# Optimization experiments

Measured on AMD Instinct MI355X. Metric: run time of the kernel, lower is better.

Reference implementation:

```python
import jax, jax.numpy as jnp
import numpy as np

VOCAB = 100000
DIM = 128
BATCH = 65536
N_NEG = 10


def setup_inputs() -> dict:
    key = jax.random.key(0)
    k1, k2, k3, k4, k5 = jax.random.split(key, 5)
    return {
        "pos_u": jax.random.randint(k1, (BATCH,), 0, VOCAB),
        "pos_v": jax.random.randint(k2, (BATCH,), 0, VOCAB),
        "neg_v": jax.random.randint(k3, (BATCH, N_NEG), 0, VOCAB),
        "u_weight": 0.01 * jax.random.normal(k4, (VOCAB, DIM), dtype=jnp.float32),
        "v_weight": 0.01 * jax.random.normal(k5, (VOCAB, DIM), dtype=jnp.float32),
    }


def reference(pos_u, pos_v, neg_v, u_weight, v_weight):
    emb_u = u_weight[pos_u]            # [B, D]
    emb_v = v_weight[pos_v]            # [B, D]
    emb_neg_v = v_weight[neg_v]        # [B, N, D]

    score = jnp.sum(emb_u * emb_v, axis=1)
    score = jnp.clip(score, -10.0, 10.0)
    score = -jax.nn.log_sigmoid(score)           # [B]

    neg_dots = jnp.einsum("bd,bnd->bn", emb_u, emb_neg_v)  # [B, N]
    # NOTE: faithful to source: neg term is ADDED (not negated) to the loss
    neg_score = jnp.sum(jax.nn.log_sigmoid(-neg_dots), axis=1)  # [B]

    return jnp.mean(score + neg_score)
```

## Files before the change

### kernel.cpp

```cpp
#include <hip/hip_runtime.h>
#include <hip/hip_fp8.h>

#define VOCAB 100000
#define DIM 128
#define BATCH 65536
#define N_NEG 10

#define BLOCKS (BATCH / 64)
#define QSCALE 256.0f
#define QINV   (1.0f / 256.0f)

typedef float v4f __attribute__((ext_vector_type(4)));
typedef int   v4i __attribute__((ext_vector_type(4)));
typedef int   v2i __attribute__((ext_vector_type(2)));
typedef float v2f __attribute__((ext_vector_type(2)));

#if __has_builtin(__builtin_amdgcn_cvt_pk_fp8_f32) && __has_builtin(__builtin_amdgcn_cvt_pk_f32_fp8)
__device__ __forceinline__ unsigned int pack4_fp8(float a, float b, float c, float d) {
    int r = __builtin_amdgcn_cvt_pk_fp8_f32(a, b, 0, false);
    r = __builtin_amdgcn_cvt_pk_fp8_f32(c, d, r, true);
    return (unsigned int)r;
}
#else
__device__ __forceinline__ unsigned int pack4_fp8(float a, float b, float c, float d) {
    unsigned int r =  (unsigned int)__hip_fp8_e4m3(a).__x;
    r |= (unsigned int)__hip_fp8_e4m3(b).__x << 8;
    r |= (unsigned int)__hip_fp8_e4m3(c).__x << 16;
    r |= (unsigned int)__hip_fp8_e4m3(d).__x << 24;
    return r;
}
#endif

#if __has_builtin(__builtin_amdgcn_cvt_pk_f32_fp8)
__device__ __forceinline__ void fma4_fp8(float& s, unsigned int x, const float* u) {
    v2f lo = __builtin_amdgcn_cvt_pk_f32_fp8(x, false);
    v2f hi = __builtin_amdgcn_cvt_pk_f32_fp8(x, true);
    s += u[0] * lo.x + u[1] * lo.y + u[2] * hi.x + u[3] * hi.y;
}
#else
__device__ __forceinline__ float fp8_to_f(unsigned int b) {
    __hip_fp8_e4m3 t; t.__x = (__hip_fp8_storage_t)b; return (float)t;
}
__device__ __forceinline__ void fma4_fp8(float& s, unsigned int x, const float* u) {
    s += u[0] * fp8_to_f(x & 0xffu) + u[1] * fp8_to_f((x >> 8) & 0xffu)
       + u[2] * fp8_to_f((x >> 16) & 0xffu) + u[3] * fp8_to_f(x >> 24);
}
#endif

__device__ __forceinline__ float dot16_fp8(uint4 w, const float* uf) {
    float s = 0.0f;
    fma4_fp8(s, w.x, uf + 0);
    fma4_fp8(s, w.y, uf + 4);
    fma4_fp8(s, w.z, uf + 8);
    fma4_fp8(s, w.w, uf + 12);
    return s;
}

__device__ __forceinline__ float softplus_log2(float x) {
    const float y = x * 1.44269504f;
    const float t = __builtin_amdgcn_exp2f(-fabsf(y));
    return fmaxf(y, 0.0f) + __builtin_amdgcn_logf(1.0f + t);
}

__global__ void zero_out_kernel(float* out) { out[0] = 0.0f; }

__global__ __launch_bounds__(256) void quantize_v_kernel(
    const float4* __restrict__ in, uint4* __restrict__ out, float* __restrict__ loss_out) {
    const int i = blockIdx.x * 256 + threadIdx.x;
    if (i == 0) loss_out[0] = 0.0f;
    const float4 a = in[i * 4 + 0];
    const float4 b = in[i * 4 + 1];
    const float4 c = in[i * 4 + 2];
    const float4 d = in[i * 4 + 3];
    uint4 r;
    r.x = pack4_fp8(a.x * QSCALE, a.y * QSCALE, a.z * QSCALE, a.w * QSCALE);
    r.y = pack4_fp8(b.x * QSCALE, b.y * QSCALE, b.z * QSCALE, b.w * QSCALE);
    r.z = pack4_fp8(c.x * QSCALE, c.y * QSCALE, c.z * QSCALE, c.w * QSCALE);
    r.w = pack4_fp8(d.x * QSCALE, d.y * QSCALE, d.z * QSCALE, d.w * QSCALE);
    out[i] = r;
}

__global__ __launch_bounds__(256, 3) void skipgram_loss_fp8_kernel(
    const int* __restrict__ pos_u,
    const int* __restrict__ pos_v,
    const int* __restrict__ neg_v,
    const float4* __restrict__ u_weight,
    const uint4* __restrict__ v8,
    float* __restrict__ out)
{
    const int tid  = threadIdx.x;
    const int lane = tid & 63;
    const int wave = tid >> 6;
    const int sub  = lane & 7;
    const int grp  = lane >> 3;

    const int gg = (blockIdx.x * 4 + wave) * 8 + grp;
    const int b0 = gg * 2;

    const v2i pu = *(const v2i*)(pos_u + b0);
    const v2i pv = *(const v2i*)(pos_v + b0);
    const v4i* __restrict__ np = (const v4i*)(neg_v + (size_t)b0 * N_NEG);
    const v4i q0 = np[0];
    const v4i q1 = np[1];
    const v4i q2 = np[2];
    const v4i q3 = np[3];
    const v4i q4 = np[4];

    const int i0[N_NEG + 1] = { pv.x, q0.x, q0.y, q0.z, q0.w, q1.x, q1.y, q1.z, q1.w, q2.x, q2.y };
    const int i1[N_NEG + 1] = { pv.y, q2.z, q2.w, q3.x, q3.y, q3.z, q3.w, q4.x, q4.y, q4.z, q4.w };

    uint4 w0[N_NEG + 1], w1[N_NEG + 1];
    #pragma unroll
    for (int j = 0; j <= N_NEG; ++j) {
        w0[j] = v8[(size_t)i0[j] * 8 + sub];
        w1[j] = v8[(size_t)i1[j] * 8 + sub];
    }
    const float4* __restrict__ urow0 = u_weight + (size_t)pu.x * 32 + sub * 4;
    const float4* __restrict__ urow1 = u_weight + (size_t)pu.y * 32 + sub * 4;
    const float4 t00 = urow0[0];
    const float4 t01 = urow0[1];
    const float4 t02 = urow0[2];
    const float4 t03 = urow0[3];
    const float4 t10 = urow1[0];
    const float4 t11 = urow1[1];
    const float4 t12 = urow1[2];
    const float4 t13 = urow1[3];

    float uf0[16], uf1[16];
    uf0[0]  = t00.x; uf0[1]  = t00.y; uf0[2]  = t00.z; uf0[3]  = t00.w;
    uf0[4]  = t01.x; uf0[5]  = t01.y; uf0[6]  = t01.z; uf0[7]  = t01.w;
    uf0[8]  = t02.x; uf0[9]  = t02.y; uf0[10] = t02.z; uf0[11] = t02.w;
    uf0[12] = t03.x; uf0[13] = t03.y; uf0[14] = t03.z; uf0[15] = t03.w;
    uf1[0]  = t10.x; uf1[1]  = t10.y; uf1[2]  = t10.z; uf1[3]  = t10.w;
    uf1[4]  = t11.x; uf1[5]  = t11.y; uf1[6]  = t11.z; uf1[7]  = t11.w;
    uf1[8]  = t12.x; uf1[9]  = t12.y; uf1[10] = t12.z; uf1[11] = t12.w;
    uf1[12] = t13.x; uf1[13] = t13.y; uf1[14] = t13.z; uf1[15] = t13.w;

    float a0[N_NEG + 1], a1[N_NEG + 1];
    #pragma unroll
    for (int j = 0; j <= N_NEG; ++j) {
        a0[j] = dot16_fp8(w0[j], uf0);
        a1[j] = dot16_fp8(w1[j], uf1);
    }

    #pragma unroll
    for (int m = 1; m < 8; m <<= 1) {
        #pragma unroll
        for (int j = 0; j <= N_NEG; ++j) {
            a0[j] += __shfl_xor(a0[j], m, 64);
            a1[j] += __shfl_xor(a1[j], m, 64);
        }
    }

    float s0 = fminf(fmaxf(a0[0] * QINV, -10.0f), 10.0f);
    float s1 = fminf(fmaxf(a1[0] * QINV, -10.0f), 10.0f);
    float loss2 = softplus_log2(-s0) + softplus_log2(-s1);
    #pragma unroll
    for (int n = 0; n < N_NEG; ++n)
        loss2 -= softplus_log2(a0[n + 1] * QINV) + softplus_log2(a1[n + 1] * QINV);
    float loss = loss2 * 0.69314718f;

    #pragma unroll
    for (int m = 8; m < 64; m <<= 1) loss += __shfl_xor(loss, m, 64);

    __shared__ float smem[4];
    if (lane == 0) smem[wave] = loss;
    __syncthreads();
    if (tid == 0)
        atomicAdd(out, (smem[0] + smem[1] + smem[2] + smem[3]) * (1.0f / (float)BATCH));
}

__device__ __forceinline__ float dot4(float4 a, float4 b) {
    return a.x * b.x + a.y * b.y + a.z * b.z + a.w * b.w;
}

__global__ __launch_bounds__(256) void skipgram_loss_fp32_kernel(
    const int* __restrict__ pos_u,
    const int* __restrict__ pos_v,
    const int* __restrict__ neg_v,
    const float4* __restrict__ u_weight,
    const float4* __restrict__ v_weight,
    float* __restrict__ out)
{
    const int tid  = threadIdx.x;
    const int lane = tid & 63;
    const int wave = tid >> 6;
    const int sub  = lane & 7;
    const int grp  = lane >> 3;

    const int b = ((blockIdx.x * 4 + wave) * 8 + grp);

    const int iu = pos_u[b];
    const int iv = pos_v[b];

    const float4* __restrict__ urow = u_weight + iu * 32;
    float4 u0 = urow[0 * 8 + sub];
    float4 u1 = urow[1 * 8 + sub];
    float4 u2 = urow[2 * 8 + sub];
    float4 u3 = urow[3 * 8 + sub];

    const float4* __restrict__ vrow = v_weight + iv * 32;
    float p = dot4(u0, vrow[0 * 8 + sub]) + dot4(u1, vrow[1 * 8 + sub])
            + dot4(u2, vrow[2 * 8 + sub]) + dot4(u3, vrow[3 * 8 + sub]);

    float nd[N_NEG];
    #pragma unroll
    for (int n = 0; n < N_NEG; ++n) {
        const int idx = neg_v[b * N_NEG + n];
        const float4* __restrict__ wrow = v_weight + idx * 32;
        nd[n] = dot4(u0, wrow[0 * 8 + sub]) + dot4(u1, wrow[1 * 8 + sub])
              + dot4(u2, wrow[2 * 8 + sub]) + dot4(u3, wrow[3 * 8 + sub]);
    }

    #pragma unroll
    for (int m = 1; m < 8; m <<= 1) {
        p += __shfl_xor(p, m, 64);
        #pragma unroll
        for (int n = 0; n < N_NEG; ++n) nd[n] += __shfl_xor(nd[n], m, 64);
    }

    float s = fminf(fmaxf(p, -10.0f), 10.0f);
    float loss2 = softplus_log2(-s);
    #pragma unroll
    for (int n = 0; n < N_NEG; ++n) loss2 -= softplus_log2(nd[n]);
    float loss = loss2 * 0.69314718f;

    #pragma unroll
    for (int m = 8; m < 64; m <<= 1) loss += __shfl_xor(loss, m, 64);

    __shared__ float smem[4];
    if (lane == 0) smem[wave] = loss;
    __syncthreads();
    if (tid == 0)
        atomicAdd(out, (smem[0] + smem[1] + smem[2] + smem[3]) * (1.0f / (float)BATCH));
}

extern "C" void kernel_launch(void* const* d_in, const int* in_sizes, int n_in,
                              void* d_out, int out_size, void* d_ws, size_t ws_size,
                              hipStream_t stream) {
    const int*    pos_u    = (const int*)d_in[0];
    const int*    pos_v    = (const int*)d_in[1];
    const int*    neg_v    = (const int*)d_in[2];
    const float4* u_weight = (const float4*)d_in[3];
    const float4* v_weight = (const float4*)d_in[4];
    float* out = (float*)d_out;

    const size_t table_bytes = (size_t)VOCAB * DIM;
    if (ws_size >= table_bytes) {
        uint4* v8 = (uint4*)d_ws;
        const int qblocks = (VOCAB * DIM / 16) / 256;
        quantize_v_kernel<<<qblocks, 256, 0, stream>>>(v_weight, v8, out);
        skipgram_loss_fp8_kernel<<<BLOCKS, 256, 0, stream>>>(
            pos_u, pos_v, neg_v, u_weight, v8, out);
    } else {
        zero_out_kernel<<<1, 1, 0, stream>>>(out);
        skipgram_loss_fp32_kernel<<<BATCH / 32, 256, 0, stream>>>(
            pos_u, pos_v, neg_v, u_weight, v_weight, out);
    }
}
```

Before: 140.1 us.

## Prefetch gathered u rows and index arrays into cache during quantize kernel

Adds extra blocks to the quantize kernel that touch the u_weight rows selected by pos_u, plus the neg_v, pos_u and pos_v index arrays, and discard the loaded values. The aim is to warm the large last-level cache so the main loss kernel's gathers and index loads hit in cache rather than HBM. This costs extra memory traffic and blocks in the first kernel, and it only pays off if the data stays resident between the two launches.

```diff
diff --git a/kernel.cpp b/kernel.cpp
--- a/kernel.cpp
+++ b/kernel.cpp
@@ -9,6 +9,12 @@
 #define BLOCKS (BATCH / 64)
 #define QSCALE 256.0f
 #define QINV   (1.0f / 256.0f)
+
+#define QBLOCKS      3125
+#define PF_U_BLOCKS  1024
+#define PF_NEG_BLOCKS 160
+#define PF_POS_BLOCKS  32
+#define QTOTAL (QBLOCKS + PF_U_BLOCKS + PF_NEG_BLOCKS + PF_POS_BLOCKS)
 
 typedef float v4f __attribute__((ext_vector_type(4)));
 typedef int   v4i __attribute__((ext_vector_type(4)));
@@ -65,19 +71,57 @@
 __global__ void zero_out_kernel(float* out) { out[0] = 0.0f; }
 
 __global__ __launch_bounds__(256) void quantize_v_kernel(
-    const float4* __restrict__ in, uint4* __restrict__ out, float* __restrict__ loss_out) {
-    const int i = blockIdx.x * 256 + threadIdx.x;
-    if (i == 0) loss_out[0] = 0.0f;
-    const float4 a = in[i * 4 + 0];
-    const float4 b = in[i * 4 + 1];
-    const float4 c = in[i * 4 + 2];
-    const float4 d = in[i * 4 + 3];
-    uint4 r;
-    r.x = pack4_fp8(a.x * QSCALE, a.y * QSCALE, a.z * QSCALE, a.w * QSCALE);
-    r.y = pack4_fp8(b.x * QSCALE, b.y * QSCALE, b.z * QSCALE, b.w * QSCALE);
-    r.z = pack4_fp8(c.x * QSCALE, c.y * QSCALE, c.z * QSCALE, c.w * QSCALE);
-    r.w = pack4_fp8(d.x * QSCALE, d.y * QSCALE, d.z * QSCALE, d.w * QSCALE);
-    out[i] = r;
+    const float4* __restrict__ in, uint4* __restrict__ out, float* __restrict__ loss_out,
+    const int* __restrict__ pos_u, const int* __restrict__ pos_v,
+    const int* __restrict__ neg_v, const float4* __restrict__ u_weight)
+{
+    const int bid = blockIdx.x;
+    const int tid = threadIdx.x;
+
+    if (bid < QBLOCKS) {
+        const int i = bid * 256 + tid;
+        if (i == 0) loss_out[0] = 0.0f;
+        const float4 a = in[i * 4 + 0];
+        const float4 b = in[i * 4 + 1];
+        const float4 c = in[i * 4 + 2];
+        const float4 d = in[i * 4 + 3];
+        uint4 r;
+        r.x = pack4_fp8(a.x * QSCALE, a.y * QSCALE, a.z * QSCALE, a.w * QSCALE);
+        r.y = pack4_fp8(b.x * QSCALE, b.y * QSCALE, b.z * QSCALE, b.w * QSCALE);
+        r.z = pack4_fp8(c.x * QSCALE, c.y * QSCALE, c.z * QSCALE, c.w * QSCALE);
+        r.w = pack4_fp8(d.x * QSCALE, d.y * QSCALE, d.z * QSCALE, d.w * QSCALE);
+        out[i] = r;
+        return;
+    }
+
+    if (bid < QBLOCKS + PF_U_BLOCKS) {
+        const int g = (bid - QBLOCKS) * 256 + tid;
+        const int elem = g >> 2;
+        const int q    = g & 3;
+        const float4* __restrict__ p = u_weight + (size_t)pos_u[elem] * 32 + q * 8;
+        float acc = p[0].x + p[1].x + p[2].x + p[3].x
+                  + p[4].x + p[5].x + p[6].x + p[7].x;
+        asm volatile("" :: "v"(acc));
+        return;
+    }
+
+    if (bid < QBLOCKS + PF_U_BLOCKS + PF_NEG_BLOCKS) {
+        const int g = (bid - QBLOCKS - PF_U_BLOCKS) * 256 + tid;
+        const uint4* __restrict__ p = (const uint4*)neg_v + (size_t)g * 4;
+        const uint4 a = p[0], b = p[1], c = p[2], d = p[3];
+        unsigned int acc = a.x + b.x + c.x + d.x;
+        asm volatile("" :: "v"(acc));
+        return;
+    }
+
+    {
+        const int g = (bid - QBLOCKS - PF_U_BLOCKS - PF_NEG_BLOCKS) * 256 + tid;
+        const uint4* __restrict__ a = (const uint4*)pos_u + (size_t)g * 2;
+        const uint4* __restrict__ b = (const uint4*)pos_v + (size_t)g * 2;
+        const uint4 x0 = a[0], x1 = a[1], y0 = b[0], y1 = b[1];
+        unsigned int acc = x0.x + x1.x + y0.x + y1.x;
+        asm volatile("" :: "v"(acc));
+    }
 }
 
 __global__ __launch_bounds__(256, 3) void skipgram_loss_fp8_kernel(
@@ -248,8 +292,8 @@
     const size_t table_bytes = (size_t)VOCAB * DIM;
     if (ws_size >= table_bytes) {
         uint4* v8 = (uint4*)d_ws;
-        const int qblocks = (VOCAB * DIM / 16) / 256;
-        quantize_v_kernel<<<qblocks, 256, 0, stream>>>(v_weight, v8, out);
+        quantize_v_kernel<<<QTOTAL, 256, 0, stream>>>(
+            v_weight, v8, out, pos_u, pos_v, neg_v, u_weight);
         skipgram_loss_fp8_kernel<<<BLOCKS, 256, 0, stream>>>(
             pos_u, pos_v, neg_v, u_weight, v8, out);
     } else {
```

Result: slower. 149.8 us (+6.9%).
